# Kernel optimization log

Measured on AMD Instinct MI355X. Metric: run time of the kernel, lower is better.

## Reference

```python
import jax, jax.numpy as jnp
import numpy as np

N = 100000
E = 1000000
C = 64      # hidden_channels
H = 4       # heads
O = C // H  # out channels per head
NEG_SLOPE = 0.2


def setup_inputs() -> dict:
    key = jax.random.key(0)
    ks = jax.random.split(key, 14)
    x = jax.random.normal(ks[0], (N, C), dtype=jnp.float32)
    edge_index = jax.random.randint(ks[1], (2, E), 0, N, dtype=jnp.int64)
    s = 1.0 / np.sqrt(C)
    params = {}
    for l in range(3):
        params[f"Wl{l+1}"] = jax.random.normal(ks[2 + 4 * l], (C, H * O), dtype=jnp.float32) * s
        params[f"Wr{l+1}"] = jax.random.normal(ks[3 + 4 * l], (C, H * O), dtype=jnp.float32) * s
        params[f"a{l+1}"] = jax.random.normal(ks[4 + 4 * l], (H, O), dtype=jnp.float32) * s
        params[f"b{l+1}"] = jnp.zeros((H * O,), dtype=jnp.float32)
    return {"x": x, "edge_index": edge_index, **params}


def _gatv2_layer(x, src, dst, Wl, Wr, a, b):
    # x: [N, C]; src/dst: [E]
    xl = (x @ Wl).reshape(N, H, O)  # source-side transform
    xr = (x @ Wr).reshape(N, H, O)  # target-side transform
    s = jax.nn.leaky_relu(xl[src] + xr[dst], NEG_SLOPE)     # [E, H, O]
    e = jnp.einsum("eho,ho->eh", s, a)                       # [E, H] logits
    # segment softmax over incoming edges of each target node
    m = jax.ops.segment_max(e, dst, num_segments=N)          # [N, H]
    ex = jnp.exp(e - m[dst])
    denom = jax.ops.segment_sum(ex, dst, num_segments=N)     # [N, H]
    alpha = ex / (denom[dst] + 1e-16)                        # [E, H]
    out = jax.ops.segment_sum(xl[src] * alpha[:, :, None], dst, num_segments=N)
    return out.reshape(N, H * O) + b


def reference(x, edge_index, Wl1, Wr1, a1, b1, Wl2, Wr2, a2, b2, Wl3, Wr3, a3, b3):
    src, dst = edge_index[0], edge_index[1]
    h = jax.nn.relu(_gatv2_layer(x, src, dst, Wl1, Wr1, a1, b1))
    h = jax.nn.relu(_gatv2_layer(h, src, dst, Wl2, Wr2, a2, b2))
    h = _gatv2_layer(h, src, dst, Wl3, Wr3, a3, b3)
    return h
```

## Files before the change

kernel.cpp:

```cpp
#include <hip/hip_runtime.h>
#include <math.h>

#define SLOPE 0.2f
#define LOG2E 1.4426950408889634f

#define DPP_ADD(x, ctrl) \
    ((x) + __int_as_float(__builtin_amdgcn_update_dpp( \
        0, __float_as_int(x), (ctrl), 0xF, 0xF, true)))


#define NPB 256
#define EPB 8192
#define MAXBK 2048

__global__ __launch_bounds__(256) void kH1(const int* __restrict__ ei,
                                           int* __restrict__ hist,
                                           int E, int nbk, int nblkE) {
    __shared__ int h[MAXBK];
    int t = threadIdx.x, b = blockIdx.x;
    for (int i = t; i < nbk; i += 256) h[i] = 0;
    __syncthreads();
    int e0 = b * EPB, e1 = min(e0 + EPB, E);
    for (int e = e0 + t; e < e1; e += 256)
        atomicAdd(&h[ei[E + e] >> 8], 1);
    __syncthreads();
    for (int i = t; i < nbk; i += 256)
        hist[i * nblkE + b] = h[i];
}

__global__ __launch_bounds__(256) void kH2(const int* __restrict__ ei,
                                           const int* __restrict__ hs,
                                           int* __restrict__ pairs,
                                           int E, int nbk, int nblkE) {
    __shared__ int soff[MAXBK];
    int t = threadIdx.x, b = blockIdx.x;
    for (int i = t; i < nbk; i += 256) soff[i] = hs[i * nblkE + b];
    __syncthreads();
    int e0 = b * EPB, e1 = min(e0 + EPB, E);
    for (int e = e0 + t; e < e1; e += 256) {
        int s = ei[e], d = ei[E + e];
        int slot = atomicAdd(&soff[d >> 8], 1);
        pairs[slot] = (s << 8) | (d & (NPB - 1));
    }
}

__global__ __launch_bounds__(256) void kB3(const int* __restrict__ hs,
                                           const int* __restrict__ pairs,
                                           int* __restrict__ btot,
                                           int E, int nbk, int nblkE) {
    __shared__ int sdeg[NPB];
    __shared__ int red[256];
    int t = threadIdx.x, b = blockIdx.x;
    sdeg[t] = 0;
    __syncthreads();
    int s0 = hs[b * nblkE];
    int s1 = (b + 1 < nbk) ? hs[(b + 1) * nblkE] : E;
    for (int i = s0 + t; i < s1; i += 256)
        atomicAdd(&sdeg[pairs[i] & (NPB - 1)], 1);
    __syncthreads();
    red[t] = (sdeg[t] + 15) & ~15;
    __syncthreads();
    for (int off = 128; off; off >>= 1) {
        if (t < off) red[t] += red[t + off];
        __syncthreads();
    }
    if (t == 0) btot[b] = red[0];
}

__global__ __launch_bounds__(256) void kscanB(const int* __restrict__ btot,
                                              int* __restrict__ bbase, int nbk) {
    __shared__ int sd[256];
    __shared__ int carry;
    int t = threadIdx.x;
    if (t == 0) carry = 0;
    __syncthreads();
    for (int base = 0; base < nbk; base += 256) {
        int v = (base + t < nbk) ? btot[base + t] : 0;
        sd[t] = v;
        __syncthreads();
        for (int off = 1; off < 256; off <<= 1) {
            int x = (t >= off) ? sd[t - off] : 0;
            __syncthreads();
            sd[t] += x;
            __syncthreads();
        }
        if (base + t < nbk) bbase[base + t] = sd[t] - v + carry;
        __syncthreads();
        if (t == 255) carry += sd[255];
        __syncthreads();
    }
}

__global__ __launch_bounds__(256) void kB4(const int* __restrict__ hs,
                                           const int* __restrict__ pairs,
                                           const int* __restrict__ bbase,
                                           int* __restrict__ rp,
                                           int* __restrict__ deg,
                                           int* __restrict__ col,
                                           int E, int nbk, int nblkE, int n) {
    __shared__ int sdeg[NPB];
    __shared__ int spfx[NPB];
    int t = threadIdx.x, b = blockIdx.x;
    sdeg[t] = 0;
    __syncthreads();
    int s0 = hs[b * nblkE];
    int s1 = (b + 1 < nbk) ? hs[(b + 1) * nblkE] : E;
    for (int i = s0 + t; i < s1; i += 256)
        atomicAdd(&sdeg[pairs[i] & (NPB - 1)], 1);
    __syncthreads();
    int cnt = sdeg[t];
    int pv = (cnt + 15) & ~15;
    spfx[t] = pv;
    __syncthreads();
    for (int off = 1; off < 256; off <<= 1) {
        int x = (t >= off) ? spfx[t - off] : 0;
        __syncthreads();
        spfx[t] += x;
        __syncthreads();
    }
    int rpt = bbase[b] + spfx[t] - pv;
    int node = b * NPB + t;
    if (node < n) { rp[node] = rpt; deg[node] = cnt; }
    __syncthreads();
    sdeg[t] = rpt;
    __syncthreads();
    for (int i = s0 + t; i < s1; i += 256) {
        int p = pairs[i];
        int slot = atomicAdd(&sdeg[p & (NPB - 1)], 1);
        col[slot] = p & ~(NPB - 1);
    }
    if (node < n)
        for (int i = rpt + cnt; i < rpt + pv; i++) col[i] = 0;
}


__global__ __launch_bounds__(256) void k_scan1(const int* __restrict__ deg,
                                               int* __restrict__ rp,
                                               int* __restrict__ blk, int n) {
    __shared__ int sd[256];
    int t = threadIdx.x;
    int base = blockIdx.x * 1024 + t * 4;
    int v0 = 0, v1 = 0, v2 = 0, v3 = 0;
    if (base + 0 < n) v0 = deg[base + 0];
    if (base + 1 < n) v1 = deg[base + 1];
    if (base + 2 < n) v2 = deg[base + 2];
    if (base + 3 < n) v3 = deg[base + 3];
    int s = v0 + v1 + v2 + v3;
    sd[t] = s;
    __syncthreads();
    for (int off = 1; off < 256; off <<= 1) {
        int x = (t >= off) ? sd[t - off] : 0;
        __syncthreads();
        sd[t] += x;
        __syncthreads();
    }
    int ex = sd[t] - s;
    if (t == 255) blk[blockIdx.x] = sd[255];
    if (base + 0 < n) rp[base + 0] = ex; ex += v0;
    if (base + 1 < n) rp[base + 1] = ex; ex += v1;
    if (base + 2 < n) rp[base + 2] = ex; ex += v2;
    if (base + 3 < n) rp[base + 3] = ex;
}

__global__ __launch_bounds__(256) void k_scan2(int* __restrict__ blk, int nblk) {
    __shared__ int sd[256];
    int t = threadIdx.x;
    int v = (t < nblk) ? blk[t] : 0;
    sd[t] = v;
    __syncthreads();
    for (int off = 1; off < 256; off <<= 1) {
        int x = (t >= off) ? sd[t - off] : 0;
        __syncthreads();
        sd[t] += x;
        __syncthreads();
    }
    if (t < nblk) blk[t] = sd[t] - v;
}

__global__ __launch_bounds__(256) void k_scan3(int* __restrict__ rp,
                                               const int* __restrict__ blk,
                                               int n) {
    int t = threadIdx.x;
    int base = blockIdx.x * 1024 + t * 4;
    int off = blk[blockIdx.x];
    #pragma unroll
    for (int i = 0; i < 4; i++) {
        int idx = base + i;
        if (idx < n) rp[idx] += off;
    }
}


__global__ __launch_bounds__(256) void k_gemm(const float* __restrict__ in,
                                              const float* __restrict__ Wl,
                                              const float* __restrict__ Wr,
                                              float* __restrict__ xl,
                                              float* __restrict__ xr, int n) {
    __shared__ float4 sW[64 * 32];
    __shared__ float  sx[128 * 68];

    int t = threadIdx.x;
    int base = blockIdx.x * 128;

    float4 xs[8];
    int xrow[8], xkq[8];
    #pragma unroll
    for (int s = 0; s < 8; s++) {
        int i = t + 256 * s;
        int row = i >> 4, kq = i & 15;
        int g = base + row;
        if (g > n - 1) g = n - 1;
        xs[s] = *(const float4*)(in + (size_t)g * 64 + kq * 4);
        xrow[s] = row; xkq[s] = kq;
    }
    for (int i = t; i < 2048; i += 256) {
        int k = i >> 5, jg = i & 31;
        const float* src = (jg < 16) ? (Wl + k * 64 + jg * 4)
                                     : (Wr + k * 64 + (jg - 16) * 4);
        sW[i] = *(const float4*)src;
    }
    #pragma unroll
    for (int s = 0; s < 8; s++)
        *(float4*)(sx + xrow[s] * 68 + xkq[s] * 4) = xs[s];
    __syncthreads();

    int rt = t & 15;
    int ct = t >> 4;
    const float* sxp = sx + rt * 68;

    float4 acc[8][2];
    #pragma unroll
    for (int r = 0; r < 8; r++) {
        acc[r][0] = make_float4(0.f, 0.f, 0.f, 0.f);
        acc[r][1] = make_float4(0.f, 0.f, 0.f, 0.f);
    }

    #pragma unroll 1
    for (int k0 = 0; k0 < 64; k0 += 4) {
        float4 xv[8];
        #pragma unroll
        for (int r = 0; r < 8; r++)
            xv[r] = *(const float4*)(sxp + r * (16 * 68) + k0);
        #pragma unroll
        for (int kk = 0; kk < 4; kk++) {
            float4 w0 = sW[(k0 + kk) * 32 + ct * 2 + 0];
            float4 w1 = sW[(k0 + kk) * 32 + ct * 2 + 1];
            #pragma unroll
            for (int r = 0; r < 8; r++) {
                float xk = (kk == 0) ? xv[r].x : (kk == 1) ? xv[r].y
                         : (kk == 2) ? xv[r].z : xv[r].w;
                acc[r][0].x += xk * w0.x;
                acc[r][0].y += xk * w0.y;
                acc[r][0].z += xk * w0.z;
                acc[r][0].w += xk * w0.w;
                acc[r][1].x += xk * w1.x;
                acc[r][1].y += xk * w1.y;
                acc[r][1].z += xk * w1.z;
                acc[r][1].w += xk * w1.w;
            }
        }
    }

    float* outh = (ct < 8) ? xl : xr;
    int cq = (ct & 7) * 8;
    #pragma unroll
    for (int r = 0; r < 8; r++) {
        int g = base + rt + 16 * r;
        if (g < n) {
            float* dst = outh + (size_t)g * 64 + cq;
            *(float4*)(dst + 0) = acc[r][0];
            *(float4*)(dst + 4) = acc[r][1];
        }
    }
}


__global__ __launch_bounds__(256) void k_node(const float* __restrict__ xl,
                                              const float* __restrict__ xr,
                                              const int* __restrict__ rp,
                                              const int* __restrict__ deg,
                                              const int* __restrict__ col,
                                              const float* __restrict__ A,
                                              const float* __restrict__ Bv,
                                              float* __restrict__ outp,
                                              int n, int relu) {
    int lane = threadIdx.x & 63;
    int node = __builtin_amdgcn_readfirstlane(blockIdx.x * 4 + (threadIdx.x >> 6));
    if (node >= n) return;
    int grp = lane >> 5;
    int s   = lane & 31;
    int chn = ((s >> 3) << 4) + ((s & 7) << 1);
    unsigned cofs = (unsigned)chn * 4u;

    float2 xr2 = *(const float2*)(xr + (size_t)node * 64 + chn);
    float2 a2  = *(const float2*)(A + chn);
    a2.x *= LOG2E; a2.y *= LOG2E;
    float2 b2  = *(const float2*)(Bv + chn);

    int start = rp[node];
    int d = deg[node];
    int nb = (d + 7) >> 3;
    const int* cp = col + start;
    const char* xlb = (const char*)xl;

    float den = 0.f;
    float ax = 0.f, ay = 0.f;

    auto batch = [&](const float2 (&v)[4], int ebase, bool full) {
        #pragma unroll
        for (int j = 0; j < 4; j++) {
            float sx_ = v[j].x + xr2.x;
            float sy_ = v[j].y + xr2.y;
            sx_ = fmaxf(sx_, SLOPE * sx_);
            sy_ = fmaxf(sy_, SLOPE * sy_);
            float q = sx_ * a2.x + sy_ * a2.y;
            q = DPP_ADD(q, 0xB1);
            q = DPP_ADD(q, 0x4E);
            q = DPP_ADD(q, 0x141);
            if (!full) {
                int eidx = ebase + 2 * j + grp;
                if (eidx >= d) q = -INFINITY;
            }
            float w = __builtin_amdgcn_exp2f(q);
            den += w;
            ax += w * v[j].x;
            ay += w * v[j].y;
        }
    };

    auto gather = [&](float2 (&v)[4], const int* q) {
        int c[8];
        *(int4*)(c + 0) = *(const int4*)(q + 0);
        *(int4*)(c + 4) = *(const int4*)(q + 4);
        #pragma unroll
        for (int j = 0; j < 4; j++) {
            unsigned cc = (unsigned)(grp ? c[2 * j + 1] : c[2 * j]);
            v[j] = *(const float2*)(xlb + (cc + cofs));
        }
    };

    float2 v[4];
    if (nb > 0) gather(v, cp);

    #pragma unroll 1
    for (int b = 0; b < nb - 1; b++) {
        float2 vN[4];
        gather(vN, cp + (b + 1) * 8);
        batch(v, b * 8, true);
        #pragma unroll
        for (int j = 0; j < 4; j++) v[j] = vN[j];
    }
    if (nb > 0) batch(v, (nb - 1) * 8, false);

    den += __shfl_xor(den, 32, 64);
    ax  += __shfl_xor(ax, 32, 64);
    ay  += __shfl_xor(ay, 32, 64);

    float inv = 1.f / (den + 1e-16f);
    float ox = ax * inv + b2.x;
    float oy = ay * inv + b2.y;
    if (relu) { ox = fmaxf(ox, 0.f); oy = fmaxf(oy, 0.f); }
    if (grp == 0)
        *(float2*)(outp + (size_t)node * 64 + chn) = make_float2(ox, oy);
}


extern "C" void kernel_launch(void* const* d_in, const int* in_sizes, int n_in,
                              void* d_out, int out_size, void* d_ws, size_t ws_size,
                              hipStream_t stream) {
    const float* x = (const float*)d_in[0];
    const int* ei = (const int*)d_in[1];
    int N = in_sizes[0] / 64;
    int E = in_sizes[1] / 2;

    const float* Wl[3] = {(const float*)d_in[2], (const float*)d_in[6], (const float*)d_in[10]};
    const float* Wr[3] = {(const float*)d_in[3], (const float*)d_in[7], (const float*)d_in[11]};
    const float* Av[3] = {(const float*)d_in[4], (const float*)d_in[8], (const float*)d_in[12]};
    const float* Bv[3] = {(const float*)d_in[5], (const float*)d_in[9], (const float*)d_in[13]};

    char* w = (char*)d_ws;
    auto carve = [&](size_t bytes) {
        void* p = (void*)w;
        w += (bytes + 255) & ~(size_t)255;
        return p;
    };
    int NBK    = (N + NPB - 1) / NPB;
    int NBLK_E = (E + EPB - 1) / EPB;
    size_t histN = (size_t)NBK * NBLK_E;
    size_t colN = (size_t)E + 15 * (size_t)N + 64;
    float* xl    = (float*)carve((size_t)N * 64 * 4);
    float* xr    = (float*)carve((size_t)N * 64 * 4);
    float* h     = (float*)carve((size_t)N * 64 * 4);
    int*   rp    = (int*)carve((size_t)N * 4);
    int*   deg   = (int*)carve((size_t)N * 4);
    int*   col   = (int*)carve(colN * 4);
    int*   pairs = (int*)carve((size_t)E * 4);
    int*   hist  = (int*)carve(histN * 4);
    int*   hs    = (int*)carve(histN * 4);
    int*   btot  = (int*)carve((size_t)NBK * 4);
    int*   bbase = (int*)carve((size_t)NBK * 4);
    int*   blkB  = (int*)carve(256 * 4);

    int nblkH1024 = (int)((histN + 1023) / 1024);
    int gemm_grid = (N + 127) / 128;
    int node_grid = (N + 3) / 4;

    kH1<<<NBLK_E, 256, 0, stream>>>(ei, hist, E, NBK, NBLK_E);
    k_scan1<<<nblkH1024, 256, 0, stream>>>(hist, hs, blkB, (int)histN);
    k_scan2<<<1, 256, 0, stream>>>(blkB, nblkH1024);
    k_scan3<<<nblkH1024, 256, 0, stream>>>(hs, blkB, (int)histN);
    kH2<<<NBLK_E, 256, 0, stream>>>(ei, hs, pairs, E, NBK, NBLK_E);

    kB3<<<NBK, 256, 0, stream>>>(hs, pairs, btot, E, NBK, NBLK_E);
    kscanB<<<1, 256, 0, stream>>>(btot, bbase, NBK);
    kB4<<<NBK, 256, 0, stream>>>(hs, pairs, bbase, rp, deg, col, E, NBK, NBLK_E, N);

    const float* in_l = x;
    for (int l = 0; l < 3; l++) {
        float* out_l = (l == 2) ? (float*)d_out : h;
        int relu = (l < 2) ? 1 : 0;
        k_gemm<<<gemm_grid, 256, 0, stream>>>(in_l, Wl[l], Wr[l], xl, xr, N);
        k_node<<<node_grid, 256, 0, stream>>>(xl, xr, rp, deg, col, Av[l], Bv[l],
                                              out_l, N, relu);
        in_l = h;
    }
}
```

Before: 375.8 us.

## Restructure projection GEMM to stream wave-uniform weights via scalar loads

Rewrites the dual projection GEMM so each wave owns one weight matrix half and each thread computes one row by 32 columns. Weights are read straight from global memory with wave-uniform addresses, so they can be served by scalar loads, instead of being staged in LDS. Only the input tile is kept in padded LDS, which shrinks the tile to 64 rows and lowers LDS use. This trades the register-blocked outer product for more per-k LDS reads and scalar-cache traffic.

```diff
diff --git a/kernel.cpp b/kernel.cpp
--- a/kernel.cpp
+++ b/kernel.cpp
@@ -196,81 +196,55 @@
                                               const float* __restrict__ Wr,
                                               float* __restrict__ xl,
                                               float* __restrict__ xr, int n) {
-    __shared__ float4 sW[64 * 32];
-    __shared__ float  sx[128 * 68];
+    __shared__ float sx[64 * 65];
 
     int t = threadIdx.x;
-    int base = blockIdx.x * 128;
-
-    float4 xs[8];
-    int xrow[8], xkq[8];
+    int base = blockIdx.x * 64;
+
     #pragma unroll
-    for (int s = 0; s < 8; s++) {
+    for (int s = 0; s < 4; s++) {
         int i = t + 256 * s;
         int row = i >> 4, kq = i & 15;
         int g = base + row;
         if (g > n - 1) g = n - 1;
-        xs[s] = *(const float4*)(in + (size_t)g * 64 + kq * 4);
-        xrow[s] = row; xkq[s] = kq;
-    }
-    for (int i = t; i < 2048; i += 256) {
-        int k = i >> 5, jg = i & 31;
-        const float* src = (jg < 16) ? (Wl + k * 64 + jg * 4)
-                                     : (Wr + k * 64 + (jg - 16) * 4);
-        sW[i] = *(const float4*)src;
-    }
+        float4 v = *(const float4*)(in + (size_t)g * 64 + kq * 4);
+        float* p = sx + row * 65 + kq * 4;
+        p[0] = v.x; p[1] = v.y; p[2] = v.z; p[3] = v.w;
+    }
+    __syncthreads();
+
+    int row = t & 63;
+    int w = __builtin_amdgcn_readfirstlane(t >> 6);
+    const float* Wp = (w < 2) ? Wl : Wr;
+    int col0 = (w & 1) * 32;
+
+    float acc[32];
     #pragma unroll
-    for (int s = 0; s < 8; s++)
-        *(float4*)(sx + xrow[s] * 68 + xkq[s] * 4) = xs[s];
-    __syncthreads();
-
-    int rt = t & 15;
-    int ct = t >> 4;
-    const float* sxp = sx + rt * 68;
-
-    float4 acc[8][2];
-    #pragma unroll
-    for (int r = 0; r < 8; r++) {
-        acc[r][0] = make_float4(0.f, 0.f, 0.f, 0.f);
-        acc[r][1] = make_float4(0.f, 0.f, 0.f, 0.f);
-    }
+    for (int j = 0; j < 32; j++) acc[j] = 0.f;
+
+    const float* sxr = sx + row * 65;
 
     #pragma unroll 1
     for (int k0 = 0; k0 < 64; k0 += 4) {
-        float4 xv[8];
-        #pragma unroll
-        for (int r = 0; r < 8; r++)
-            xv[r] = *(const float4*)(sxp + r * (16 * 68) + k0);
         #pragma unroll
         for (int kk = 0; kk < 4; kk++) {
-            float4 w0 = sW[(k0 + kk) * 32 + ct * 2 + 0];
-            float4 w1 = sW[(k0 + kk) * 32 + ct * 2 + 1];
+            int k = k0 + kk;
+            float xk = sxr[k];
+            const float* wrow = Wp + k * 64 + col0;
             #pragma unroll
-            for (int r = 0; r < 8; r++) {
-                float xk = (kk == 0) ? xv[r].x : (kk == 1) ? xv[r].y
-                         : (kk == 2) ? xv[r].z : xv[r].w;
-                acc[r][0].x += xk * w0.x;
-                acc[r][0].y += xk * w0.y;
-                acc[r][0].z += xk * w0.z;
-                acc[r][0].w += xk * w0.w;
-                acc[r][1].x += xk * w1.x;
-                acc[r][1].y += xk * w1.y;
-                acc[r][1].z += xk * w1.z;
-                acc[r][1].w += xk * w1.w;
-            }
+            for (int j = 0; j < 32; j++)
+                acc[j] = fmaf(wrow[j], xk, acc[j]);
         }
     }
 
-    float* outh = (ct < 8) ? xl : xr;
-    int cq = (ct & 7) * 8;
-    #pragma unroll
-    for (int r = 0; r < 8; r++) {
-        int g = base + rt + 16 * r;
-        if (g < n) {
-            float* dst = outh + (size_t)g * 64 + cq;
-            *(float4*)(dst + 0) = acc[r][0];
-            *(float4*)(dst + 4) = acc[r][1];
-        }
+    float* outh = (w < 2) ? xl : xr;
+    int g = base + row;
+    if (g < n) {
+        float* dst = outh + (size_t)g * 64 + col0;
+        #pragma unroll
+        for (int j = 0; j < 32; j += 4)
+            *(float4*)(dst + j) =
+                make_float4(acc[j], acc[j + 1], acc[j + 2], acc[j + 3]);
     }
 }
 
@@ -402,7 +376,7 @@
     int*   blkB  = (int*)carve(256 * 4);
 
     int nblkH1024 = (int)((histN + 1023) / 1024);
-    int gemm_grid = (N + 127) / 128;
+    int gemm_grid = (N + 63) / 64;
     int node_grid = (N + 3) / 4;
 
     kH1<<<NBLK_E, 256, 0, stream>>>(ei, hist, E, NBK, NBLK_E);
```

Measured after the change: 393.5 us. +4.7%, slower.
